# Kernel optimization log

Hardware: AMD Instinct MI355X
Metric: run time of the kernel (lower is better)

The kernel has to match this reference:

```python
import jax, jax.numpy as jnp
import numpy as np

BSZ, L, D, K = 4, 4096, 512, 4


def setup_inputs() -> dict:
    key = jax.random.key(0)
    ks = jax.random.split(key, 8)
    n = jnp.arange(D, dtype=jnp.float32)
    f = jnp.sqrt(2.0 * n + 1.0)
    f = f / f.max()
    omega = jnp.exp(-f * np.float32(np.log(10000.0)))  # hippo_freqs(D)
    # freqs are strictly decreasing in n -> argsort descending == arange
    band_idx = jnp.argsort(-omega).reshape(K, D // K).astype(jnp.int32)
    B_vec = jnp.sqrt(2.0 * n + 1.0)
    B_vec = B_vec / B_vec.max()  # hippo_b_vector(D)
    return {
        "x": jax.random.normal(ks[0], (BSZ, L, D), dtype=jnp.float32),
        "z_prev": jax.random.normal(ks[1], (BSZ, L, D), dtype=jnp.float32),
        "W_psi": jax.random.normal(ks[2], (2 * D, D), dtype=jnp.float32) * 0.02,
        "b_psi": jnp.zeros((2 * D,), jnp.float32),
        "W_phi": jax.random.normal(ks[3], (2 * D, D), dtype=jnp.float32) * 0.02,
        "b_phi": jnp.zeros((2 * D,), jnp.float32),
        "W_gate": jax.random.normal(ks[4], (1, D), dtype=jnp.float32) * 0.02,
        "b_gate": jnp.zeros((1,), jnp.float32),
        "omega": omega,
        "log_gamma": jax.random.normal(ks[5], (D,), dtype=jnp.float32) - 3.0,
        "dt": jnp.array(0.1, jnp.float32),
        "surprise_gain": jnp.zeros((1,), jnp.float32),
        "tau": jnp.ones((1,), jnp.float32),
        "beta": jnp.zeros((1,), jnp.float32),
        "B_vec": B_vec,
        "band_idx": band_idx,
    }


def _exact_projection(z):
    # geodesic projection to zero-mean unit-std along last axis
    m = z.mean(-1, keepdims=True)
    v = ((z - m) ** 2).mean(-1, keepdims=True)
    return (z - m) / (jnp.sqrt(v) + 1e-6)


def reference(x, z_prev, W_psi, b_psi, W_phi, b_phi, W_gate, b_gate,
              omega, log_gamma, dt, surprise_gain, tau, beta, B_vec, band_idx):
    B_, L_, D_ = x.shape
    K_ = band_idx.shape[0]

    psi_raw = x @ W_psi.T + b_psi          # [B,L,2D]
    psi = jax.lax.complex(psi_raw[..., :D_], psi_raw[..., D_:])
    phi_raw = x @ W_phi.T + b_phi
    phi = jax.lax.complex(phi_raw[..., :D_], phi_raw[..., D_:])

    gate = jax.nn.sigmoid(x @ W_gate.T + b_gate)          # [B,L,1]
    surprise = jnp.abs(x - z_prev).mean(-1, keepdims=True)
    gate = gate * (1.0 + jnp.tanh(surprise_gain) * surprise)

    U = (gate * B_vec).astype(jnp.complex64) * psi        # [B,L,D] complex

    dta = jnp.abs(dt)
    lam = jax.lax.complex(-jnp.exp(log_gamma), omega)     # [D]
    t = jnp.arange(L_, dtype=jnp.float32)
    kernel = jnp.exp(lam[None, :] * (t[:, None] * dta))   # [L,D] complex, A^t

    n_fft = 2 * L_
    K_freq = jnp.fft.fft(kernel.T, n=n_fft, axis=1)                 # [D,2L]
    U_freq = jnp.fft.fft(jnp.transpose(U, (0, 2, 1)), n=n_fft, axis=2)  # [B,D,2L]
    H = jnp.fft.ifft(U_freq * K_freq[None], axis=2)[:, :, :L_]
    H = jnp.transpose(H, (0, 2, 1))                        # [B,L,D] complex

    H_proj = jax.lax.complex(_exact_projection(H.real), _exact_projection(H.imag))

    Hb = H_proj[:, :, band_idx]   # [B,L,K,band]
    Pb = phi[:, :, band_idx]
    alpha = (jnp.conj(Hb) * Pb).sum(-1, keepdims=True) / (D_ // K_)  # [B,L,K,1]
    c_k = jax.nn.softmax(jnp.abs(alpha) / jnp.clip(tau, 1e-4, None), axis=2)
    alpha_ig = alpha * c_k * K_
    density = (Hb.real ** 2 + Hb.imag ** 2).mean(-1, keepdims=True)
    alpha_fin = alpha_ig + (beta * density).astype(alpha_ig.dtype)
    out_bands = (Hb * alpha_fin).real                      # [B,L,K,band]

    out = jnp.zeros((B_, L_, D_), x.dtype).at[:, :, band_idx].set(out_bands)
    return out
```

## Files before the change

kernel.cpp:

```cpp
#include <hip/hip_runtime.h>
#include <hip/hip_bf16.h>
#include <math.h>

#define BSZ   4
#define LSEQ  4096
#define DDIM  512
#define KBAND 4
#define MROWS (BSZ*LSEQ)
#define BLD   (MROWS*DDIM)
#define CHUNK 16
#define NCH   (LSEQ/CHUNK)
#define NGRP  16
#define TBL   ((CHUNK+1)*DDIM)
#define NCOLS 2048

typedef __attribute__((ext_vector_type(8))) short  short8;
typedef __attribute__((ext_vector_type(8))) unsigned short u16x8;
typedef __attribute__((ext_vector_type(4))) unsigned short u16x4;
typedef __attribute__((ext_vector_type(4))) float  f32x4;

__device__ __forceinline__ unsigned short f2bf(float f) {
    unsigned int u = __float_as_uint(f);
    u = (u + 0x7FFFu + ((u >> 16) & 1u)) >> 16;
    return (unsigned short)u;
}
__device__ __forceinline__ float bf2f(unsigned short h) {
    return __uint_as_float(((unsigned int)h) << 16);
}

__device__ __forceinline__ void gld_lds16(const void* g, void* l) {
    __builtin_amdgcn_global_load_lds(
        (const __attribute__((address_space(1))) void*)g,
        (__attribute__((address_space(3))) void*)l, 16, 0, 0);
}

__global__ void k_prep(const float* __restrict__ omega,
                       const float* __restrict__ log_gamma,
                       const float* __restrict__ dt,
                       const int*   __restrict__ band_idx,
                       float* __restrict__ apR, float* __restrict__ apI,
                       float* __restrict__ apgR, float* __restrict__ apgI,
                       int* __restrict__ bandOf, int* __restrict__ posOf)
{
    int gid = blockIdx.x * blockDim.x + threadIdx.x;
    float dta = fabsf(dt[0]);
    if (gid < TBL) {
        int k = gid / DDIM, d = gid % DDIM;
        float g = -expf(log_gamma[d]);
        float w = omega[d];
        float e = expf(g * dta * (float)k);
        float s, c;
        sincosf(w * dta * (float)k, &s, &c);
        apR[gid] = e * c;
        apI[gid] = e * s;
    } else if (gid < 2*TBL) {
        int gg = gid - TBL;
        int k = gg / DDIM, d = gg % DDIM;
        float g = -expf(log_gamma[d]);
        float w = omega[d];
        float ph = dta * (float)(16 * k);
        float e = expf(g * ph);
        float s, c;
        sincosf(w * ph, &s, &c);
        apgR[gg] = e * c;
        apgI[gg] = e * s;
    }
    if (gid < DDIM) {
        int d = band_idx[gid];
        bandOf[d] = gid >> 7;
        posOf[d]  = gid & 127;
    }
}

__global__ void k_cvtgate(const float* __restrict__ x,
                          const float* __restrict__ z_prev,
                          const float* __restrict__ Wg,
                          const float* __restrict__ bg,
                          const float* __restrict__ sg,
                          float* __restrict__ gate,
                          unsigned short* __restrict__ Ahi,
                          unsigned short* __restrict__ Alo)
{
    int m    = blockIdx.x * 4 + (threadIdx.x >> 6);
    int lane = threadIdx.x & 63;
    const float4* xr = (const float4*)(x      + ((size_t)m << 9));
    const float4* zr = (const float4*)(z_prev + ((size_t)m << 9));
    const float4* wg = (const float4*)Wg;
    float dot = 0.f, sur = 0.f;
    int msw = m & 7;
#pragma unroll
    for (int i = 0; i < 2; i++) {
        int e = lane + i*64;
        float4 a = xr[e];
        float4 z = zr[e];
        float4 w = wg[e];
        dot += a.x*w.x + a.y*w.y + a.z*w.z + a.w*w.w;
        sur += fabsf(a.x-z.x) + fabsf(a.y-z.y) + fabsf(a.z-z.z) + fabsf(a.w-z.w);
        float fa[4] = {a.x, a.y, a.z, a.w};
        u16x4 h, l;
#pragma unroll
        for (int j = 0; j < 4; ++j) {
            unsigned short hb = f2bf(fa[j]);
            h[j] = hb;
            l[j] = f2bf(fa[j] - bf2f(hb));
        }
        int grp = e >> 1, half = e & 1;
        int chunk = grp >> 3, gs = grp & 7;
        int gd = gs ^ msw;
        size_t dst = ((size_t)m << 9) + chunk*64 + gd*8 + half*4;
        *(u16x4*)(Ahi + dst) = h;
        *(u16x4*)(Alo + dst) = l;
    }
#pragma unroll
    for (int mm = 32; mm; mm >>= 1) { dot += __shfl_xor(dot, mm); sur += __shfl_xor(sur, mm); }
    if (lane == 0) {
        float g = 1.f / (1.f + expf(-(dot + bg[0])));
        g *= (1.f + tanhf(sg[0]) * (sur * (1.f/512.f)));
        gate[m] = g;
    }
}

__global__ void k_cvtB(const float* __restrict__ Wpsi,
                       const float* __restrict__ Wphi,
                       unsigned short* __restrict__ Bhi,
                       unsigned short* __restrict__ Blo)
{
    int gid = blockIdx.x * 256 + threadIdx.x;
    int n = gid >> 6, grp = gid & 63;
    int chunk = grp >> 3, g = grp & 7;
    int se = chunk*64 + ((g ^ (n & 7)) << 3);
    const float* wp = (n < 1024) ? (Wpsi + ((size_t)n << 9) + se)
                                 : (Wphi + ((size_t)(n - 1024) << 9) + se);
    u16x8 h, l;
#pragma unroll
    for (int j = 0; j < 8; ++j) {
        float f = wp[j];
        unsigned short hb = f2bf(f);
        h[j] = hb;
        l[j] = f2bf(f - bf2f(hb));
    }
    size_t dst = ((size_t)n << 9) + grp*8;
    *(u16x8*)(Bhi + dst) = h;
    *(u16x8*)(Blo + dst) = l;
}

__global__ __launch_bounds__(256)
void k_gemm_bf16(const unsigned short* __restrict__ Ahi,
                 const unsigned short* __restrict__ Alo,
                 const unsigned short* __restrict__ Bhi,
                 const unsigned short* __restrict__ Blo,
                 const float* __restrict__ bpsi, const float* __restrict__ bphi,
                 float* __restrict__ psiR, float* __restrict__ psiI,
                 float* __restrict__ phiR, float* __restrict__ phiI)
{
    __shared__ __align__(16) char As[16384];
    __shared__ __align__(16) char Bs[16384];

    int bid = blockIdx.x;
    int wg  = (bid & 7) * 256 + (bid >> 3);
    int m0 = (wg >> 4) * 128;
    int n0 = (wg & 15) * 128;

    int tid  = threadIdx.x;
    int lane = tid & 63;
    int wv   = tid >> 6;
    int wm = wv >> 1, wn = wv & 1;
    int lr = lane & 15, lk = lane >> 4;

    f32x4 acc[4][4];
#pragma unroll
    for (int mi = 0; mi < 4; ++mi)
#pragma unroll
        for (int ni = 0; ni < 4; ++ni) acc[mi][ni] = (f32x4)0.f;

    for (int s = 0; s < 24; ++s) {
        const unsigned short* Asrc = (s >= 8 && s < 16) ? Alo : Ahi;
        const unsigned short* Bsrc = (s < 16) ? Bhi : Blo;
        int kb2 = (s & 7) << 7;

        __syncthreads();
#pragma unroll
        for (int i = 0; i < 4; ++i) {
            int flat = tid + i * 256;
            int r = flat >> 3, g = flat & 7;
            size_t goff = ((size_t)r << 10) + kb2 + g * 16;
            gld_lds16((const char*)Asrc + ((size_t)m0 << 10) + goff,
                      As + (wv * 64 + i * 256) * 16);
            gld_lds16((const char*)Bsrc + ((size_t)n0 << 10) + goff,
                      Bs + (wv * 64 + i * 256) * 16);
        }
        __syncthreads();

#pragma unroll
        for (int kk = 0; kk < 2; ++kk) {
            int tb = (kk * 64 + lk * 16) ^ ((lr & 7) << 4);
            short8 af[4], bfr[4];
#pragma unroll
            for (int mi = 0; mi < 4; ++mi) {
                int r = wm * 64 + mi * 16 + lr;
                af[mi] = *(const short8*)(As + r * 128 + tb);
            }
#pragma unroll
            for (int ni = 0; ni < 4; ++ni) {
                int r = wn * 64 + ni * 16 + lr;
                bfr[ni] = *(const short8*)(Bs + r * 128 + tb);
            }
#pragma unroll
            for (int mi = 0; mi < 4; ++mi)
#pragma unroll
                for (int ni = 0; ni < 4; ++ni)
                    acc[mi][ni] = __builtin_amdgcn_mfma_f32_16x16x32_bf16(
                        af[mi], bfr[ni], acc[mi][ni], 0, 0, 0);
        }
    }

#pragma unroll
    for (int ni = 0; ni < 4; ++ni) {
        int ncol = n0 + wn * 64 + ni * 16 + lr;
        float bias = (ncol < 1024) ? bpsi[ncol] : bphi[ncol - 1024];
        int p = ncol >> 9;
        float* plane = (p == 0) ? psiR : (p == 1) ? psiI : (p == 2) ? phiR : phiI;
        int col = ncol & 511;
#pragma unroll
        for (int mi = 0; mi < 4; ++mi) {
            int mrow = m0 + wm * 64 + mi * 16 + lk * 4;
#pragma unroll
            for (int j = 0; j < 4; ++j)
                plane[(size_t)(mrow + j) * 512 + col] = acc[mi][ni][j] + bias;
        }
    }
}

__launch_bounds__(512)
__global__ void k_scan(float* __restrict__ HR, float* __restrict__ HI,
                       const float* __restrict__ gate,
                       const float* __restrict__ Bvec,
                       const float* __restrict__ apR, const float* __restrict__ apI,
                       float* __restrict__ carR, float* __restrict__ carI)
{
    int b = blockIdx.x >> 8;
    int c = blockIdx.x & 255;
    int d = threadIdx.x;
    float ar = apR[DDIM + d], ai = apI[DDIM + d];
    float bv = Bvec[d];
    float hr = 0.f, hi = 0.f;
    int t0 = c * CHUNK;
    size_t base = ((size_t)b * LSEQ + t0) * DDIM + d;
    const float* grow = gate + (size_t)b * LSEQ + t0;
#pragma unroll
    for (int t = 0; t < CHUNK; t++) {
        float pr = HR[base], pi = HI[base];
        float g  = grow[t] * bv;
        float ur = g * pr, ui = g * pi;
        float nr = ar*hr - ai*hi + ur;
        float ni = ar*hi + ai*hr + ui;
        hr = nr; hi = ni;
        HR[base] = hr; HI[base] = hi;
        base += DDIM;
    }
    size_t ci = ((size_t)(b * NCH + c)) * DDIM + d;
    carR[ci] = hr; carI[ci] = hi;
}

__global__ void k_carryA(float* __restrict__ carR, float* __restrict__ carI,
                         const float* __restrict__ apR, const float* __restrict__ apI)
{
    int gid = blockIdx.x * 256 + threadIdx.x;
    int d = gid & 511, cg = (gid >> 9) & 15, b = gid >> 13;
    float qr = apR[CHUNK*DDIM + d], qi = apI[CHUNK*DDIM + d];
    size_t i0 = ((size_t)(b * NCH + cg * 16)) * DDIM + d;
    float cr = carR[i0], ci = carI[i0];
#pragma unroll
    for (int j = 1; j < 16; j++) {
        float xr = carR[i0 + (size_t)j * DDIM];
        float xi = carI[i0 + (size_t)j * DDIM];
        float nr = qr*cr - qi*ci + xr;
        float ni = qr*ci + qi*cr + xi;
        cr = nr; ci = ni;
        carR[i0 + (size_t)j * DDIM] = cr;
        carI[i0 + (size_t)j * DDIM] = ci;
    }
}

__global__ void k_carryB(const float* __restrict__ carR, const float* __restrict__ carI,
                         const float* __restrict__ apgR, const float* __restrict__ apgI,
                         float* __restrict__ gcarR, float* __restrict__ gcarI)
{
    int gid = blockIdx.x * 256 + threadIdx.x;
    int d = gid & 511, b = gid >> 9;
    float Qr = apgR[16*DDIM + d], Qi = apgI[16*DDIM + d];
    size_t base = ((size_t)(b * NCH + 15)) * DDIM + d;
    float gr = carR[base], gi = carI[base];
    gcarR[((size_t)(b*NGRP))*DDIM + d] = gr;
    gcarI[((size_t)(b*NGRP))*DDIM + d] = gi;
#pragma unroll
    for (int cg = 1; cg < NGRP; cg++) {
        size_t idx = ((size_t)(b * NCH + cg*16 + 15)) * DDIM + d;
        float tr = carR[idx], ti = carI[idx];
        float nr = Qr*gr - Qi*gi + tr;
        float ni = Qr*gi + Qi*gr + ti;
        gr = nr; gi = ni;
        gcarR[((size_t)(b*NGRP + cg))*DDIM + d] = gr;
        gcarI[((size_t)(b*NGRP + cg))*DDIM + d] = gi;
    }
}

__global__ void k_carryC(float* __restrict__ carR, float* __restrict__ carI,
                         const float* __restrict__ apgR, const float* __restrict__ apgI,
                         const float* __restrict__ gcarR, const float* __restrict__ gcarI)
{
    int gid = blockIdx.x * 256 + threadIdx.x;
    int d = gid & 511, c = (gid >> 9) & 255, b = gid >> 17;
    int cg = c >> 4;
    if (cg == 0) return;
    int jj = c & 15;
    float fr = apgR[(jj+1)*DDIM + d], fi = apgI[(jj+1)*DDIM + d];
    size_t gidx = ((size_t)(b*NGRP + cg - 1))*DDIM + d;
    float gr = gcarR[gidx], gi = gcarI[gidx];
    size_t idx = ((size_t)(b * NCH + c)) * DDIM + d;
    carR[idx] += fr*gr - fi*gi;
    carI[idx] += fr*gi + fi*gr;
}

__device__ __forceinline__ float2 blockSum2(float a, float b, float* red)
{
#pragma unroll
    for (int m = 32; m; m >>= 1) { a += __shfl_xor(a, m); b += __shfl_xor(b, m); }
    int tid = threadIdx.x, w = tid >> 6;
    if ((tid & 63) == 0) { red[w*2] = a; red[w*2+1] = b; }
    __syncthreads();
    a = 0.f; b = 0.f;
#pragma unroll
    for (int i = 0; i < 8; i++) { a += red[i*2]; b += red[i*2+1]; }
    __syncthreads();
    return make_float2(a, b);
}

__launch_bounds__(512)
__global__ void k_out(const float* __restrict__ HR, const float* __restrict__ HI,
                      const float* __restrict__ phR, const float* __restrict__ phI,
                      const float* __restrict__ carR, const float* __restrict__ carI,
                      const float* __restrict__ apR, const float* __restrict__ apI,
                      const int* __restrict__ bandOf, const int* __restrict__ posOf,
                      const float* __restrict__ tau, const float* __restrict__ beta,
                      float* __restrict__ out)
{
    __shared__ float sA[512], sB[512], sC[512];
    __shared__ float pA[8], pB[8], pC[8];
    __shared__ float red[16];

    int bt = blockIdx.x;
    int b = bt >> 12, t = bt & 4095;
    int d = threadIdx.x;
    size_t idx = (size_t)bt * DDIM + d;

    float hr = HR[idx], hi = HI[idx];
    int c = t >> 4, off = t & 15;
    if (c > 0) {
        size_t ci = ((size_t)(b * NCH + (c - 1))) * DDIM + d;
        float cr = carR[ci], cm = carI[ci];
        float pr = apR[(off + 1) * DDIM + d], pi = apI[(off + 1) * DDIM + d];
        hr += pr*cr - pi*cm;
        hi += pr*cm + pi*cr;
    }
    float2 s = blockSum2(hr, hi, red);
    float mr = s.x * (1.f/512.f), mi = s.y * (1.f/512.f);
    float dr = hr - mr, di = hi - mi;
    float2 v = blockSum2(dr*dr, di*di, red);
    float Hpr = dr / (sqrtf(v.x * (1.f/512.f)) + 1e-6f);
    float Hpi = di / (sqrtf(v.y * (1.f/512.f)) + 1e-6f);

    float pr_ = phR[idx], pi_ = phI[idx];
    float ar_ = Hpr*pr_ + Hpi*pi_;
    float ai_ = Hpr*pi_ - Hpi*pr_;
    float dn_ = Hpr*Hpr + Hpi*Hpi;

    int kb = bandOf[d], jb = posOf[d];
    sA[kb*128 + jb] = ar_;
    sB[kb*128 + jb] = ai_;
    sC[kb*128 + jb] = dn_;
    __syncthreads();

    float v0 = sA[d], v1 = sB[d], v2 = sC[d];
#pragma unroll
    for (int m = 32; m; m >>= 1) {
        v0 += __shfl_xor(v0, m); v1 += __shfl_xor(v1, m); v2 += __shfl_xor(v2, m);
    }
    int w = d >> 6;
    if ((d & 63) == 0) { pA[w] = v0; pB[w] = v1; pC[w] = v2; }
    __syncthreads();

    float tv = tau[0]; tv = (tv < 1e-4f) ? 1e-4f : tv;
    float bt_s = beta[0];
    float aRk[4], aIk[4], dnk[4], mag[4];
    float mx = -1e30f;
#pragma unroll
    for (int k = 0; k < 4; k++) {
        aRk[k] = (pA[2*k] + pA[2*k+1]) * (1.f/128.f);
        aIk[k] = (pB[2*k] + pB[2*k+1]) * (1.f/128.f);
        dnk[k] = (pC[2*k] + pC[2*k+1]) * (1.f/128.f);
        mag[k] = sqrtf(aRk[k]*aRk[k] + aIk[k]*aIk[k]) / tv;
        mx = fmaxf(mx, mag[k]);
    }
    float se = 0.f, ek[4];
#pragma unroll
    for (int k = 0; k < 4; k++) { ek[k] = expf(mag[k] - mx); se += ek[k]; }
    float inv = 1.f / se;

    int kd = kb;
    float ck  = ek[kd] * inv;
    float afR = aRk[kd] * ck * 4.f + bt_s * dnk[kd];
    float afI = aIk[kd] * ck * 4.f;
    out[idx] = Hpr * afR - Hpi * afI;
}

extern "C" void kernel_launch(void* const* d_in, const int* in_sizes, int n_in,
                              void* d_out, int out_size, void* d_ws, size_t ws_size,
                              hipStream_t stream)
{
    const float* x        = (const float*)d_in[0];
    const float* z_prev   = (const float*)d_in[1];
    const float* W_psi    = (const float*)d_in[2];
    const float* b_psi    = (const float*)d_in[3];
    const float* W_phi    = (const float*)d_in[4];
    const float* b_phi    = (const float*)d_in[5];
    const float* W_gate   = (const float*)d_in[6];
    const float* b_gate   = (const float*)d_in[7];
    const float* omega    = (const float*)d_in[8];
    const float* log_gam  = (const float*)d_in[9];
    const float* dt       = (const float*)d_in[10];
    const float* sg       = (const float*)d_in[11];
    const float* tau      = (const float*)d_in[12];
    const float* beta     = (const float*)d_in[13];
    const float* B_vec    = (const float*)d_in[14];
    const int*   band_idx = (const int*)d_in[15];
    float* out = (float*)d_out;
    float* ws  = (float*)d_ws;

    float* psiR = ws;
    float* psiI = psiR + BLD;
    float* phiR = psiI + BLD;
    float* phiI = phiR + BLD;
    float* gate = phiI + BLD;
    float* apR  = gate + MROWS;
    float* apI  = apR + TBL;
    float* apgR = apI + TBL;
    float* apgI = apgR + TBL;
    float* carR = apgI + TBL;
    float* carI = carR + (size_t)BSZ*NCH*DDIM;
    float* gcarR = carI + (size_t)BSZ*NCH*DDIM;
    float* gcarI = gcarR + (size_t)BSZ*NGRP*DDIM;
    int* bandOf = (int*)(gcarI + (size_t)BSZ*NGRP*DDIM);
    int* posOf  = bandOf + DDIM;
    unsigned short* Bhi = (unsigned short*)(posOf + DDIM);
    unsigned short* Blo = Bhi + (size_t)NCOLS*512;

    unsigned short* Ahi = (unsigned short*)d_out;
    unsigned short* Alo = Ahi + (size_t)MROWS*512;

    k_prep<<<(2*TBL + 255)/256, 256, 0, stream>>>(
        omega, log_gam, dt, band_idx, apR, apI, apgR, apgI, bandOf, posOf);

    k_cvtgate<<<MROWS/4, 256, 0, stream>>>(x, z_prev, W_gate, b_gate, sg,
                                           gate, Ahi, Alo);

    k_cvtB<<<(NCOLS*64)/256, 256, 0, stream>>>(W_psi, W_phi, Bhi, Blo);

    k_gemm_bf16<<<(MROWS/128) * (NCOLS/128), 256, 0, stream>>>(
        Ahi, Alo, Bhi, Blo, b_psi, b_phi, psiR, psiI, phiR, phiI);

    k_scan<<<BSZ * NCH, 512, 0, stream>>>(psiR, psiI, gate, B_vec, apR, apI, carR, carI);

    k_carryA<<<(BSZ*NGRP*DDIM)/256, 256, 0, stream>>>(carR, carI, apR, apI);
    k_carryB<<<(BSZ*DDIM)/256, 256, 0, stream>>>(carR, carI, apgR, apgI, gcarR, gcarI);
    k_carryC<<<(BSZ*NCH*DDIM)/256, 256, 0, stream>>>(carR, carI, apgR, apgI, gcarR, gcarI);

    k_out<<<MROWS, 512, 0, stream>>>(psiR, psiI, phiR, phiI, carR, carI,
                                     apR, apI, bandOf, posOf, tau, beta, out);
}
```

Before: 412.5 us.

## Batch four rows per block in output kernel and prefetch scan loads

The output kernel now handles four sequence positions per 512-thread block. Its block reductions are batched so that barriers and the carry load are shared across those rows, and a quarter as many blocks are launched. The scan and carry kernels first load their chunk values into register arrays, then compute the recurrence, then store, so the loads are issued together instead of serialized behind the dependency chain. The cost is more registers and shared memory per block, which may lower occupancy.

```diff
diff --git a/kernel.cpp b/kernel.cpp
--- a/kernel.cpp
+++ b/kernel.cpp
@@ -243,20 +243,29 @@
     int d = threadIdx.x;
     float ar = apR[DDIM + d], ai = apI[DDIM + d];
     float bv = Bvec[d];
-    float hr = 0.f, hi = 0.f;
     int t0 = c * CHUNK;
     size_t base = ((size_t)b * LSEQ + t0) * DDIM + d;
     const float* grow = gate + (size_t)b * LSEQ + t0;
+
+    float ur[CHUNK], ui[CHUNK];
 #pragma unroll
     for (int t = 0; t < CHUNK; t++) {
-        float pr = HR[base], pi = HI[base];
+        ur[t] = HR[base + (size_t)t * DDIM];
+        ui[t] = HI[base + (size_t)t * DDIM];
+    }
+    float hr = 0.f, hi = 0.f;
+#pragma unroll
+    for (int t = 0; t < CHUNK; t++) {
         float g  = grow[t] * bv;
-        float ur = g * pr, ui = g * pi;
-        float nr = ar*hr - ai*hi + ur;
-        float ni = ar*hi + ai*hr + ui;
+        float nr = ar*hr - ai*hi + g * ur[t];
+        float ni = ar*hi + ai*hr + g * ui[t];
         hr = nr; hi = ni;
-        HR[base] = hr; HI[base] = hi;
-        base += DDIM;
+        ur[t] = hr; ui[t] = hi;
+    }
+#pragma unroll
+    for (int t = 0; t < CHUNK; t++) {
+        HR[base + (size_t)t * DDIM] = ur[t];
+        HI[base + (size_t)t * DDIM] = ui[t];
     }
     size_t ci = ((size_t)(b * NCH + c)) * DDIM + d;
     carR[ci] = hr; carI[ci] = hi;
@@ -269,16 +278,24 @@
     int d = gid & 511, cg = (gid >> 9) & 15, b = gid >> 13;
     float qr = apR[CHUNK*DDIM + d], qi = apI[CHUNK*DDIM + d];
     size_t i0 = ((size_t)(b * NCH + cg * 16)) * DDIM + d;
+    float xr[15], xi[15];
+#pragma unroll
+    for (int j = 1; j < 16; j++) {
+        xr[j-1] = carR[i0 + (size_t)j * DDIM];
+        xi[j-1] = carI[i0 + (size_t)j * DDIM];
+    }
     float cr = carR[i0], ci = carI[i0];
 #pragma unroll
     for (int j = 1; j < 16; j++) {
-        float xr = carR[i0 + (size_t)j * DDIM];
-        float xi = carI[i0 + (size_t)j * DDIM];
-        float nr = qr*cr - qi*ci + xr;
-        float ni = qr*ci + qi*cr + xi;
+        float nr = qr*cr - qi*ci + xr[j-1];
+        float ni = qr*ci + qi*cr + xi[j-1];
         cr = nr; ci = ni;
-        carR[i0 + (size_t)j * DDIM] = cr;
-        carI[i0 + (size_t)j * DDIM] = ci;
+        xr[j-1] = cr; xi[j-1] = ci;
+    }
+#pragma unroll
+    for (int j = 1; j < 16; j++) {
+        carR[i0 + (size_t)j * DDIM] = xr[j-1];
+        carI[i0 + (size_t)j * DDIM] = xi[j-1];
     }
 }
 
@@ -289,16 +306,19 @@
     int gid = blockIdx.x * 256 + threadIdx.x;
     int d = gid & 511, b = gid >> 9;
     float Qr = apgR[16*DDIM + d], Qi = apgI[16*DDIM + d];
-    size_t base = ((size_t)(b * NCH + 15)) * DDIM + d;
-    float gr = carR[base], gi = carI[base];
+    float tr[NGRP], ti[NGRP];
+#pragma unroll
+    for (int cg = 0; cg < NGRP; cg++) {
+        size_t idx = ((size_t)(b * NCH + cg*16 + 15)) * DDIM + d;
+        tr[cg] = carR[idx]; ti[cg] = carI[idx];
+    }
+    float gr = tr[0], gi = ti[0];
     gcarR[((size_t)(b*NGRP))*DDIM + d] = gr;
     gcarI[((size_t)(b*NGRP))*DDIM + d] = gi;
 #pragma unroll
     for (int cg = 1; cg < NGRP; cg++) {
-        size_t idx = ((size_t)(b * NCH + cg*16 + 15)) * DDIM + d;
-        float tr = carR[idx], ti = carI[idx];
-        float nr = Qr*gr - Qi*gi + tr;
-        float ni = Qr*gi + Qi*gr + ti;
+        float nr = Qr*gr - Qi*gi + tr[cg];
+        float ni = Qr*gi + Qi*gr + ti[cg];
         gr = nr; gi = ni;
         gcarR[((size_t)(b*NGRP + cg))*DDIM + d] = gr;
         gcarI[((size_t)(b*NGRP + cg))*DDIM + d] = gi;
@@ -322,20 +342,6 @@
     carI[idx] += fr*gi + fi*gr;
 }
 
-__device__ __forceinline__ float2 blockSum2(float a, float b, float* red)
-{
-#pragma unroll
-    for (int m = 32; m; m >>= 1) { a += __shfl_xor(a, m); b += __shfl_xor(b, m); }
-    int tid = threadIdx.x, w = tid >> 6;
-    if ((tid & 63) == 0) { red[w*2] = a; red[w*2+1] = b; }
-    __syncthreads();
-    a = 0.f; b = 0.f;
-#pragma unroll
-    for (int i = 0; i < 8; i++) { a += red[i*2]; b += red[i*2+1]; }
-    __syncthreads();
-    return make_float2(a, b);
-}
-
 __launch_bounds__(512)
 __global__ void k_out(const float* __restrict__ HR, const float* __restrict__ HI,
                       const float* __restrict__ phR, const float* __restrict__ phI,
@@ -345,73 +351,127 @@
                       const float* __restrict__ tau, const float* __restrict__ beta,
                       float* __restrict__ out)
 {
-    __shared__ float sA[512], sB[512], sC[512];
-    __shared__ float pA[8], pB[8], pC[8];
-    __shared__ float red[16];
-
-    int bt = blockIdx.x;
-    int b = bt >> 12, t = bt & 4095;
+    __shared__ float sA[4][512], sB[4][512], sC[4][512];
+    __shared__ float pA[4][8], pB[4][8], pC[4][8];
+    __shared__ float red[8][8];
+
+    int bt0 = blockIdx.x * 4;
+    int b = bt0 >> 12, t0 = bt0 & 4095;
     int d = threadIdx.x;
-    size_t idx = (size_t)bt * DDIM + d;
-
-    float hr = HR[idx], hi = HI[idx];
-    int c = t >> 4, off = t & 15;
+    int w = d >> 6, lane = d & 63;
+    int c = t0 >> 4, off0 = t0 & 15;
+
+    float hr[4], hi[4];
+#pragma unroll
+    for (int r = 0; r < 4; ++r) {
+        size_t idx = ((size_t)(bt0 + r) << 9) + d;
+        hr[r] = HR[idx]; hi[r] = HI[idx];
+    }
     if (c > 0) {
         size_t ci = ((size_t)(b * NCH + (c - 1))) * DDIM + d;
         float cr = carR[ci], cm = carI[ci];
-        float pr = apR[(off + 1) * DDIM + d], pi = apI[(off + 1) * DDIM + d];
-        hr += pr*cr - pi*cm;
-        hi += pr*cm + pi*cr;
-    }
-    float2 s = blockSum2(hr, hi, red);
-    float mr = s.x * (1.f/512.f), mi = s.y * (1.f/512.f);
-    float dr = hr - mr, di = hi - mi;
-    float2 v = blockSum2(dr*dr, di*di, red);
-    float Hpr = dr / (sqrtf(v.x * (1.f/512.f)) + 1e-6f);
-    float Hpi = di / (sqrtf(v.y * (1.f/512.f)) + 1e-6f);
-
-    float pr_ = phR[idx], pi_ = phI[idx];
-    float ar_ = Hpr*pr_ + Hpi*pi_;
-    float ai_ = Hpr*pi_ - Hpi*pr_;
-    float dn_ = Hpr*Hpr + Hpi*Hpi;
+#pragma unroll
+        for (int r = 0; r < 4; ++r) {
+            float pr = apR[(off0 + r + 1) * DDIM + d];
+            float pi = apI[(off0 + r + 1) * DDIM + d];
+            hr[r] += pr*cr - pi*cm;
+            hi[r] += pr*cm + pi*cr;
+        }
+    }
+
+    float sh[4], si[4];
+#pragma unroll
+    for (int r = 0; r < 4; ++r) { sh[r] = hr[r]; si[r] = hi[r]; }
+#pragma unroll
+    for (int m = 32; m; m >>= 1)
+#pragma unroll
+        for (int r = 0; r < 4; ++r) { sh[r] += __shfl_xor(sh[r], m); si[r] += __shfl_xor(si[r], m); }
+    if (lane == 0)
+#pragma unroll
+        for (int r = 0; r < 4; ++r) { red[w][2*r] = sh[r]; red[w][2*r+1] = si[r]; }
+    __syncthreads();
+    float mr[4], mi[4];
+#pragma unroll
+    for (int r = 0; r < 4; ++r) {
+        float a = 0.f, bb = 0.f;
+#pragma unroll
+        for (int ww = 0; ww < 8; ++ww) { a += red[ww][2*r]; bb += red[ww][2*r+1]; }
+        mr[r] = a * (1.f/512.f); mi[r] = bb * (1.f/512.f);
+    }
+    __syncthreads();
+
+    float dr[4], di[4];
+#pragma unroll
+    for (int r = 0; r < 4; ++r) {
+        dr[r] = hr[r] - mr[r]; di[r] = hi[r] - mi[r];
+        sh[r] = dr[r]*dr[r];   si[r] = di[r]*di[r];
+    }
+#pragma unroll
+    for (int m = 32; m; m >>= 1)
+#pragma unroll
+        for (int r = 0; r < 4; ++r) { sh[r] += __shfl_xor(sh[r], m); si[r] += __shfl_xor(si[r], m); }
+    if (lane == 0)
+#pragma unroll
+        for (int r = 0; r < 4; ++r) { red[w][2*r] = sh[r]; red[w][2*r+1] = si[r]; }
+    __syncthreads();
+    float Hpr[4], Hpi[4];
+#pragma unroll
+    for (int r = 0; r < 4; ++r) {
+        float a = 0.f, bb = 0.f;
+#pragma unroll
+        for (int ww = 0; ww < 8; ++ww) { a += red[ww][2*r]; bb += red[ww][2*r+1]; }
+        Hpr[r] = dr[r] / (sqrtf(a * (1.f/512.f)) + 1e-6f);
+        Hpi[r] = di[r] / (sqrtf(bb * (1.f/512.f)) + 1e-6f);
+    }
+    __syncthreads();
 
     int kb = bandOf[d], jb = posOf[d];
-    sA[kb*128 + jb] = ar_;
-    sB[kb*128 + jb] = ai_;
-    sC[kb*128 + jb] = dn_;
+    int sidx = kb*128 + jb;
+#pragma unroll
+    for (int r = 0; r < 4; ++r) {
+        size_t idx = ((size_t)(bt0 + r) << 9) + d;
+        float pr_ = phR[idx], pi_ = phI[idx];
+        sA[r][sidx] = Hpr[r]*pr_ + Hpi[r]*pi_;
+        sB[r][sidx] = Hpr[r]*pi_ - Hpi[r]*pr_;
+        sC[r][sidx] = Hpr[r]*Hpr[r] + Hpi[r]*Hpi[r];
+    }
     __syncthreads();
 
-    float v0 = sA[d], v1 = sB[d], v2 = sC[d];
-#pragma unroll
-    for (int m = 32; m; m >>= 1) {
-        v0 += __shfl_xor(v0, m); v1 += __shfl_xor(v1, m); v2 += __shfl_xor(v2, m);
-    }
-    int w = d >> 6;
-    if ((d & 63) == 0) { pA[w] = v0; pB[w] = v1; pC[w] = v2; }
+#pragma unroll
+    for (int r = 0; r < 4; ++r) {
+        float v0 = sA[r][d], v1 = sB[r][d], v2 = sC[r][d];
+#pragma unroll
+        for (int m = 32; m; m >>= 1) {
+            v0 += __shfl_xor(v0, m); v1 += __shfl_xor(v1, m); v2 += __shfl_xor(v2, m);
+        }
+        if (lane == 0) { pA[r][w] = v0; pB[r][w] = v1; pC[r][w] = v2; }
+    }
     __syncthreads();
 
     float tv = tau[0]; tv = (tv < 1e-4f) ? 1e-4f : tv;
     float bt_s = beta[0];
-    float aRk[4], aIk[4], dnk[4], mag[4];
-    float mx = -1e30f;
-#pragma unroll
-    for (int k = 0; k < 4; k++) {
-        aRk[k] = (pA[2*k] + pA[2*k+1]) * (1.f/128.f);
-        aIk[k] = (pB[2*k] + pB[2*k+1]) * (1.f/128.f);
-        dnk[k] = (pC[2*k] + pC[2*k+1]) * (1.f/128.f);
-        mag[k] = sqrtf(aRk[k]*aRk[k] + aIk[k]*aIk[k]) / tv;
-        mx = fmaxf(mx, mag[k]);
-    }
-    float se = 0.f, ek[4];
-#pragma unroll
-    for (int k = 0; k < 4; k++) { ek[k] = expf(mag[k] - mx); se += ek[k]; }
-    float inv = 1.f / se;
-
-    int kd = kb;
-    float ck  = ek[kd] * inv;
-    float afR = aRk[kd] * ck * 4.f + bt_s * dnk[kd];
-    float afI = aIk[kd] * ck * 4.f;
-    out[idx] = Hpr * afR - Hpi * afI;
+#pragma unroll
+    for (int r = 0; r < 4; ++r) {
+        float aRk[4], aIk[4], dnk[4], mag[4];
+        float mx = -1e30f;
+#pragma unroll
+        for (int k = 0; k < 4; k++) {
+            aRk[k] = (pA[r][2*k] + pA[r][2*k+1]) * (1.f/128.f);
+            aIk[k] = (pB[r][2*k] + pB[r][2*k+1]) * (1.f/128.f);
+            dnk[k] = (pC[r][2*k] + pC[r][2*k+1]) * (1.f/128.f);
+            mag[k] = sqrtf(aRk[k]*aRk[k] + aIk[k]*aIk[k]) / tv;
+            mx = fmaxf(mx, mag[k]);
+        }
+        float se = 0.f, ek[4];
+#pragma unroll
+        for (int k = 0; k < 4; k++) { ek[k] = expf(mag[k] - mx); se += ek[k]; }
+        float inv = 1.f / se;
+        float ck  = ek[kb] * inv;
+        float afR = aRk[kb] * ck * 4.f + bt_s * dnk[kb];
+        float afI = aIk[kb] * ck * 4.f;
+        size_t idx = ((size_t)(bt0 + r) << 9) + d;
+        out[idx] = Hpr[r] * afR - Hpi[r] * afI;
+    }
 }
 
 extern "C" void kernel_launch(void* const* d_in, const int* in_sizes, int n_in,
@@ -475,6 +535,6 @@
     k_carryB<<<(BSZ*DDIM)/256, 256, 0, stream>>>(carR, carI, apgR, apgI, gcarR, gcarI);
     k_carryC<<<(BSZ*NCH*DDIM)/256, 256, 0, stream>>>(carR, carI, apgR, apgI, gcarR, gcarI);
 
-    k_out<<<MROWS, 512, 0, stream>>>(psiR, psiI, phiR, phiI, carR, carI,
-                                     apR, apI, bandOf, posOf, tau, beta, out);
-}
+    k_out<<<MROWS/4, 512, 0, stream>>>(psiR, psiI, phiR, phiI, carR, carI,
+                                       apR, apI, bandOf, posOf, tau, beta, out);
+}
```

Measured after the change: 418.4 us. About the same (+1.4%).
